# Kernel tuning notes

Hardware: AMD Instinct MI355X
Metric: run time of the kernel (lower is better)

## Reference

```python
import jax, jax.numpy as jnp
import numpy as np


def setup_inputs() -> dict:
    key = jax.random.key(0)
    ks = jax.random.split(key, 5)
    B, NINS, NHID = 128, 4096, 128
    inputs = jax.random.normal(ks[0], (B, NINS, NHID), dtype=jnp.float32)
    claims = jax.random.normal(ks[1], (B, NHID), dtype=jnp.float32)  # unused by forward
    # project: Linear(2*nhid -> 64) -> ReLU -> Linear(64 -> 1)
    W1 = jax.random.normal(ks[2], (2 * NHID, 64), dtype=jnp.float32) * (1.0 / np.sqrt(2 * NHID))
    b1 = jnp.zeros((64,), dtype=jnp.float32)
    W2 = jax.random.normal(ks[3], (64, 1), dtype=jnp.float32) * (1.0 / np.sqrt(64))
    b2 = jnp.zeros((1,), dtype=jnp.float32)
    return {"inputs": inputs, "index": 5, "claims": claims,
            "W1": W1, "b1": b1, "W2": W2, "b2": b2}


def reference(inputs, index, claims, W1, b1, W2, b2):
    # inputs: [B, nins, nhid]
    B, NINS, NHID = inputs.shape
    own = jax.lax.dynamic_slice_in_dim(inputs, index, 1, axis=1)  # [B, 1, nhid]
    own = jnp.broadcast_to(own, (B, NINS, NHID))                  # repeat over nins
    tmp = jnp.concatenate([own, inputs], axis=2)                  # [B, nins, 2*nhid]
    h = jax.nn.relu(jnp.einsum('bnd,dk->bnk', tmp, W1) + b1)      # [B, nins, 64]
    att = jnp.einsum('bnk,ko->bno', h, W2) + b2                   # [B, nins, 1]
    weights = jax.nn.softmax(att[..., 0], axis=1)                 # [B, nins]
    outputs = jnp.einsum('bnd,bn->bd', inputs, weights)           # [B, nhid]
    return outputs
```

## Files before the change

kernel.cpp:

```cpp
#include <hip/hip_runtime.h>
#include <math.h>

#define BATCH 128
#define NINS  4096
#define NHID  128
#define KH    64
#define TILES_PER_BLOCK 2
#define NBLK_PER_B (NINS / (64 * TILES_PER_BLOCK))
#define PART_STRIDE (NHID + 2)

__global__ void precompute_c(const float* __restrict__ inputs,
                             const int* __restrict__ index_p,
                             const float* __restrict__ W1,
                             const float* __restrict__ b1,
                             float* __restrict__ c) {
    const int b = blockIdx.x;
    const int k = threadIdx.x;
    const int idx = index_p[0];
    const float* own = inputs + ((size_t)b * NINS + idx) * NHID;
    float acc = b1[k];
    for (int d = 0; d < NHID; ++d)
        acc = fmaf(own[d], W1[d * KH + k], acc);
    c[b * KH + k] = acc;
}

__global__ __launch_bounds__(64)
void att_partial(const float* __restrict__ inputs,
                 const float* __restrict__ W1,
                 const float* __restrict__ W2,
                 const float* __restrict__ b2_p,
                 const float* __restrict__ c,
                 float* __restrict__ part) {
    const int lane = threadIdx.x;
    const int b    = blockIdx.y;
    const float* Wb    = W1 + (size_t)NHID * KH;
    const float* xbase = inputs + (size_t)b * NINS * NHID;
    const float  b2v   = b2_p[0];

    float m_run = -INFINITY;
    float L_run = 0.0f;
    float o0 = 0.0f, o1 = 0.0f;

    for (int t = 0; t < TILES_PER_BLOCK; ++t) {
        const int n0 = (blockIdx.x * TILES_PER_BLOCK + t) * 64;
        const float* xrow = xbase + (size_t)(n0 + lane) * NHID;

        float h[KH];
        #pragma unroll
        for (int k = 0; k < KH; ++k) h[k] = c[b * KH + k];

        for (int dc = 0; dc < NHID; dc += 16) {
            float4 xv[4];
            #pragma unroll
            for (int i = 0; i < 4; ++i)
                xv[i] = *(const float4*)(xrow + dc + i * 4);
            const float* xs = (const float*)xv;
            #pragma unroll
            for (int i = 0; i < 16; ++i) {
                const float xd = xs[i];
                const float* wrow = Wb + (size_t)(dc + i) * KH;
                #pragma unroll
                for (int k = 0; k < KH; ++k)
                    h[k] = fmaf(xd, wrow[k], h[k]);
            }
        }

        float att = b2v;
        #pragma unroll
        for (int k = 0; k < KH; ++k)
            att = fmaf(fmaxf(h[k], 0.0f), W2[k], att);

        float m_t = att;
        #pragma unroll
        for (int off = 32; off; off >>= 1)
            m_t = fmaxf(m_t, __shfl_xor(m_t, off));

        const float M     = fmaxf(m_run, m_t);
        const float alpha = __expf(m_run - M);
        o0 *= alpha; o1 *= alpha; L_run *= alpha;

        const float e = __expf(att - M);
        float se = e;
        #pragma unroll
        for (int off = 32; off; off >>= 1)
            se += __shfl_xor(se, off);
        L_run += se;

        const float* xt = xbase + (size_t)n0 * NHID;
        for (int l = 0; l < 64; ++l) {
            const float el = __shfl(e, l);
            o0 = fmaf(el, xt[(size_t)l * NHID + lane],      o0);
            o1 = fmaf(el, xt[(size_t)l * NHID + lane + 64], o1);
        }
        m_run = M;
    }

    float* p = part + (size_t)(b * gridDim.x + blockIdx.x) * PART_STRIDE;
    if (lane == 0) { p[0] = m_run; p[1] = L_run; }
    p[2 + lane]      = o0;
    p[2 + lane + 64] = o1;
}

__global__ void finalize(const float* __restrict__ part,
                         float* __restrict__ out) {
    const int b = blockIdx.x;
    const int d = threadIdx.x;
    const float* pb = part + (size_t)b * NBLK_PER_B * PART_STRIDE;

    float M = -INFINITY;
    for (int p = 0; p < NBLK_PER_B; ++p)
        M = fmaxf(M, pb[p * PART_STRIDE]);

    float S = 0.0f, acc = 0.0f;
    for (int p = 0; p < NBLK_PER_B; ++p) {
        const float sc = __expf(pb[p * PART_STRIDE] - M);
        S   = fmaf(sc, pb[p * PART_STRIDE + 1], S);
        acc = fmaf(sc, pb[p * PART_STRIDE + 2 + d], acc);
    }
    out[b * NHID + d] = acc / S;
}

extern "C" void kernel_launch(void* const* d_in, const int* in_sizes, int n_in,
                              void* d_out, int out_size, void* d_ws, size_t ws_size,
                              hipStream_t stream) {
    const float* inputs = (const float*)d_in[0];
    const int*   index  = (const int*)  d_in[1];
    const float* W1     = (const float*)d_in[3];
    const float* b1     = (const float*)d_in[4];
    const float* W2     = (const float*)d_in[5];
    const float* b2     = (const float*)d_in[6];
    float* out = (float*)d_out;

    float* c    = (float*)d_ws;
    float* part = c + BATCH * KH;

    precompute_c<<<dim3(BATCH), dim3(64), 0, stream>>>(inputs, index, W1, b1, c);

    dim3 gB(NBLK_PER_B, BATCH);
    att_partial<<<gB, dim3(64), 0, stream>>>(inputs, W1, W2, b2, c, part);

    finalize<<<dim3(BATCH), dim3(NHID), 0, stream>>>(part, out);
}
```

Measured before the change: 455.2 us.

## Give each wave one tile in 256-thread blocks and batch weighted-sum loads

```diff
diff --git a/kernel.cpp b/kernel.cpp
--- a/kernel.cpp
+++ b/kernel.cpp
@@ -5,8 +5,7 @@
 #define NINS  4096
 #define NHID  128
 #define KH    64
-#define TILES_PER_BLOCK 2
-#define NBLK_PER_B (NINS / (64 * TILES_PER_BLOCK))
+#define NPART 64
 #define PART_STRIDE (NHID + 2)
 
 __global__ void precompute_c(const float* __restrict__ inputs,
@@ -19,84 +18,86 @@
     const int idx = index_p[0];
     const float* own = inputs + ((size_t)b * NINS + idx) * NHID;
     float acc = b1[k];
+    #pragma unroll 8
     for (int d = 0; d < NHID; ++d)
         acc = fmaf(own[d], W1[d * KH + k], acc);
     c[b * KH + k] = acc;
 }
 
-__global__ __launch_bounds__(64)
+__global__ __launch_bounds__(256)
 void att_partial(const float* __restrict__ inputs,
                  const float* __restrict__ W1,
                  const float* __restrict__ W2,
                  const float* __restrict__ b2_p,
                  const float* __restrict__ c,
                  float* __restrict__ part) {
-    const int lane = threadIdx.x;
+    const int lane = threadIdx.x & 63;
+    const int wv   = threadIdx.x >> 6;
+    const int tile = blockIdx.x * 4 + wv;
     const int b    = blockIdx.y;
+    const int n0   = tile * 64;
+
     const float* Wb    = W1 + (size_t)NHID * KH;
     const float* xbase = inputs + (size_t)b * NINS * NHID;
-    const float  b2v   = b2_p[0];
+    const float* xrow  = xbase + (size_t)(n0 + lane) * NHID;
+    const float* cb    = c + b * KH;
 
-    float m_run = -INFINITY;
-    float L_run = 0.0f;
-    float o0 = 0.0f, o1 = 0.0f;
+    float h[KH];
+    #pragma unroll
+    for (int k = 0; k < KH; ++k) h[k] = cb[k];
 
-    for (int t = 0; t < TILES_PER_BLOCK; ++t) {
-        const int n0 = (blockIdx.x * TILES_PER_BLOCK + t) * 64;
-        const float* xrow = xbase + (size_t)(n0 + lane) * NHID;
-
-        float h[KH];
+    for (int dc = 0; dc < NHID; dc += 16) {
+        float4 xv[4];
         #pragma unroll
-        for (int k = 0; k < KH; ++k) h[k] = c[b * KH + k];
-
-        for (int dc = 0; dc < NHID; dc += 16) {
-            float4 xv[4];
+        for (int i = 0; i < 4; ++i)
+            xv[i] = *(const float4*)(xrow + dc + i * 4);
+        const float* xs = (const float*)xv;
+        #pragma unroll
+        for (int i = 0; i < 16; ++i) {
+            const float xd = xs[i];
+            const float* wrow = Wb + (size_t)(dc + i) * KH;
             #pragma unroll
-            for (int i = 0; i < 4; ++i)
-                xv[i] = *(const float4*)(xrow + dc + i * 4);
-            const float* xs = (const float*)xv;
-            #pragma unroll
-            for (int i = 0; i < 16; ++i) {
-                const float xd = xs[i];
-                const float* wrow = Wb + (size_t)(dc + i) * KH;
-                #pragma unroll
-                for (int k = 0; k < KH; ++k)
-                    h[k] = fmaf(xd, wrow[k], h[k]);
-            }
+            for (int k = 0; k < KH; ++k)
+                h[k] = fmaf(xd, wrow[k], h[k]);
         }
-
-        float att = b2v;
-        #pragma unroll
-        for (int k = 0; k < KH; ++k)
-            att = fmaf(fmaxf(h[k], 0.0f), W2[k], att);
-
-        float m_t = att;
-        #pragma unroll
-        for (int off = 32; off; off >>= 1)
-            m_t = fmaxf(m_t, __shfl_xor(m_t, off));
-
-        const float M     = fmaxf(m_run, m_t);
-        const float alpha = __expf(m_run - M);
-        o0 *= alpha; o1 *= alpha; L_run *= alpha;
-
-        const float e = __expf(att - M);
-        float se = e;
-        #pragma unroll
-        for (int off = 32; off; off >>= 1)
-            se += __shfl_xor(se, off);
-        L_run += se;
-
-        const float* xt = xbase + (size_t)n0 * NHID;
-        for (int l = 0; l < 64; ++l) {
-            const float el = __shfl(e, l);
-            o0 = fmaf(el, xt[(size_t)l * NHID + lane],      o0);
-            o1 = fmaf(el, xt[(size_t)l * NHID + lane + 64], o1);
-        }
-        m_run = M;
     }
 
-    float* p = part + (size_t)(b * gridDim.x + blockIdx.x) * PART_STRIDE;
-    if (lane == 0) { p[0] = m_run; p[1] = L_run; }
+    float att = b2_p[0];
+    #pragma unroll
+    for (int k = 0; k < KH; ++k)
+        att = fmaf(fmaxf(h[k], 0.0f), W2[k], att);
+
+    float m = att;
+    #pragma unroll
+    for (int off = 32; off; off >>= 1)
+        m = fmaxf(m, __shfl_xor(m, off));
+
+    const float e = __expf(att - m);
+    float L = e;
+    #pragma unroll
+    for (int off = 32; off; off >>= 1)
+        L += __shfl_xor(L, off);
+
+    float o0 = 0.0f, o1 = 0.0f;
+    const float* xt = xbase + (size_t)n0 * NHID + lane;
+    #pragma unroll
+    for (int lb = 0; lb < 64; lb += 8) {
+        float ev[8], xa[8], xb[8];
+        #pragma unroll
+        for (int j = 0; j < 8; ++j) {
+            ev[j] = __shfl(e, lb + j);
+            xa[j] = xt[(size_t)(lb + j) * NHID];
+            xb[j] = xt[(size_t)(lb + j) * NHID + 64];
+        }
+        #pragma unroll
+        for (int j = 0; j < 8; ++j) {
+            o0 = fmaf(ev[j], xa[j], o0);
+            o1 = fmaf(ev[j], xb[j], o1);
+        }
+    }
+
+    float* p = part + (size_t)(b * NPART + tile) * PART_STRIDE;
+    if (lane == 0) { p[0] = m; p[1] = L; }
     p[2 + lane]      = o0;
     p[2 + lane + 64] = o1;
 }
@@ -105,14 +106,16 @@
                          float* __restrict__ out) {
     const int b = blockIdx.x;
     const int d = threadIdx.x;
-    const float* pb = part + (size_t)b * NBLK_PER_B * PART_STRIDE;
+    const float* pb = part + (size_t)b * NPART * PART_STRIDE;
 
     float M = -INFINITY;
-    for (int p = 0; p < NBLK_PER_B; ++p)
+    #pragma unroll 8
+    for (int p = 0; p < NPART; ++p)
         M = fmaxf(M, pb[p * PART_STRIDE]);
 
     float S = 0.0f, acc = 0.0f;
-    for (int p = 0; p < NBLK_PER_B; ++p) {
+    #pragma unroll 4
+    for (int p = 0; p < NPART; ++p) {
         const float sc = __expf(pb[p * PART_STRIDE] - M);
         S   = fmaf(sc, pb[p * PART_STRIDE + 1], S);
         acc = fmaf(sc, pb[p * PART_STRIDE + 2 + d], acc);
@@ -136,8 +139,8 @@
 
     precompute_c<<<dim3(BATCH), dim3(64), 0, stream>>>(inputs, index, W1, b1, c);
 
-    dim3 gB(NBLK_PER_B, BATCH);
-    att_partial<<<gB, dim3(64), 0, stream>>>(inputs, W1, W2, b2, c, part);
+    dim3 gB(NPART / 4, BATCH);
+    att_partial<<<gB, dim3(256), 0, stream>>>(inputs, W1, W2, b2, c, part);
 
     finalize<<<dim3(BATCH), dim3(NHID), 0, stream>>>(part, out);
 }
```

Result: slower. 542.3 us (+19.1%).
